# Optimization experiments

Measured on AMD Instinct MI355X. Metric: run time of the kernel, lower is better.

## Reference

```python
import jax, jax.numpy as jnp
import numpy as np

DT = 0.01
OMEGA_MAX = 100.0


def setup_inputs() -> dict:
    key = jax.random.key(0)
    ks = jax.random.split(key, 7)
    B, T, D, M = 4, 4096, 1024, 64
    N = 2 * M
    u = jax.random.normal(ks[0], (B, T, D), dtype=jnp.float32)
    W_omega = jax.random.normal(ks[1], (M, D), dtype=jnp.float32) * 0.02
    b_omega = jnp.ones((M,), dtype=jnp.float32)
    W_zeta = jax.random.normal(ks[2], (M, D), dtype=jnp.float32) * 0.02
    b_zeta = jnp.zeros((M,), dtype=jnp.float32)
    W_B = jax.random.normal(ks[3], (N, D), dtype=jnp.float32) * (0.1 / np.sqrt(D))
    b_B = jnp.zeros((N,), dtype=jnp.float32)
    C = jax.random.normal(ks[4], (D, N), dtype=jnp.float32) * 0.01
    D_mat = jax.random.normal(ks[5], (D, D), dtype=jnp.float32) * 0.01
    return dict(u=u, W_omega=W_omega, b_omega=b_omega, W_zeta=W_zeta,
                b_zeta=b_zeta, W_B=W_B, b_B=b_B, C=C, D_mat=D_mat)


def reference(u, W_omega, b_omega, W_zeta, b_zeta, W_B, b_B, C, D_mat):
    B, T, D = u.shape
    M = W_omega.shape[0]
    # Hoist all per-step linear projections into batched GEMMs (same math).
    omega = jax.nn.softplus(jnp.einsum('btd,md->btm', u, W_omega) + b_omega)
    omega = jnp.clip(omega, 1e-4, OMEGA_MAX)                      # (B,T,M)
    zeta = jax.nn.sigmoid(jnp.einsum('btd,md->btm', u, W_zeta) + b_zeta)
    A = omega * omega                                             # (B,T,M)
    S = 1.0 / (1.0 + (DT * DT) * A)                               # (B,T,M)
    d = 1.0 - zeta                                                # (B,T,M)
    F = jnp.einsum('btd,nd->btn', u, W_B) + b_B                   # (B,T,2M)

    def step(x, inp):
        A_t, S_t, d_t, F_t = inp                                  # (B,M)x3, (B,2M)
        z = x[:, :M]
        y = x[:, M:]
        z_new = d_t * (S_t * z - DT * A_t * S_t * y)
        y_new = d_t * (DT * S_t * z + S_t * y)
        x_new = jnp.concatenate([z_new, y_new], axis=-1) + F_t
        return x_new, x_new

    x0 = jnp.zeros((B, 2 * M), dtype=u.dtype)
    tm = lambda a: jnp.swapaxes(a, 0, 1)  # to time-major for scan
    _, xs = jax.lax.scan(step, x0, (tm(A), tm(S), tm(d), tm(F)))
    xs = jnp.swapaxes(xs, 0, 1)                                   # (B,T,2M)
    # Output projection: y_t = x_t C^T + u_t D^T
    y = jnp.einsum('btn,dn->btd', xs, C) + jnp.einsum('bte,de->btd', u, D_mat)
    return y
```

## Files before the change

kernel.cpp:

```cpp
#include <hip/hip_runtime.h>
#include <hip/hip_bf16.h>
#include <math.h>

#define DTC 0.01f

typedef __attribute__((ext_vector_type(8))) short short8;
typedef __attribute__((ext_vector_type(4))) float f32x4;
typedef unsigned short bf16raw;

__device__ __forceinline__ bf16raw f2bf(float f){
  union { unsigned u; float f; } v; v.f = f;
  unsigned r = v.u + 0x7FFF + ((v.u >> 16) & 1u);
  return (bf16raw)(r >> 16);
}

__device__ __forceinline__ short8 ld8f(const float* __restrict__ p){
  float4 a = *(const float4*)p;
  float4 b = *(const float4*)(p + 4);
  short8 r;
  r[0] = (short)f2bf(a.x); r[1] = (short)f2bf(a.y);
  r[2] = (short)f2bf(a.z); r[3] = (short)f2bf(a.w);
  r[4] = (short)f2bf(b.x); r[5] = (short)f2bf(b.y);
  r[6] = (short)f2bf(b.z); r[7] = (short)f2bf(b.w);
  return r;
}

template<int ITERS>
__device__ __forceinline__ void stage_async(const bf16raw* __restrict__ src, long ld,
                                            long row0, int k0, bf16raw* lds,
                                            int wave, int lane){
  int kchunk = (lane & 3) ^ ((lane >> 3) & 3);
#pragma unroll
  for (int i = 0; i < ITERS; ++i){
    int r0 = (wave*ITERS + i) * 16;
    long row = row0 + r0 + (lane >> 2);
    const bf16raw* gp = src + row*ld + k0 + kchunk*8;
    bf16raw* lp = lds + r0*32;
    __builtin_amdgcn_global_load_lds((const __attribute__((address_space(1))) void*)gp,
                                     (__attribute__((address_space(3))) void*)lp,
                                     16, 0, 0);
  }
}

template<int NI>
__device__ __forceinline__ void mma_tile(const bf16raw* Alds, const bf16raw* Blds,
                                         f32x4 acc[4][NI], int wm, int wn, int quad, int t16){
  short8 af[4], bfr[NI];
  int sw = (quad ^ ((t16 >> 1) & 3)) * 8;
#pragma unroll
  for (int mi = 0; mi < 4; ++mi)
    af[mi] = *(const short8*)(Alds + (wm*64 + mi*16 + t16)*32 + sw);
#pragma unroll
  for (int ni = 0; ni < NI; ++ni)
    bfr[ni] = *(const short8*)(Blds + (wn*(NI*16) + ni*16 + t16)*32 + sw);
#pragma unroll
  for (int mi = 0; mi < 4; ++mi)
#pragma unroll
    for (int ni = 0; ni < NI; ++ni)
      acc[mi][ni] = __builtin_amdgcn_mfma_f32_16x16x32_bf16(af[mi], bfr[ni], acc[mi][ni], 0, 0, 0);
}

extern "C" __global__ void k_prep(const float* __restrict__ u,
    const float* __restrict__ Wom, const float* __restrict__ Wze,
    const float* __restrict__ WB, const float* __restrict__ Cm,
    const float* __restrict__ Dm, bf16raw* __restrict__ u_bf,
    bf16raw* __restrict__ Wcat, bf16raw* __restrict__ C_bf,
    bf16raw* __restrict__ Dm_bf){
  long g = (long)blockIdx.x * 256 + threadIdx.x;
  const float* src; bf16raw* dst; long o;
  if      (g < 2097152){ src = u;   dst = u_bf;          o = g; }
  else if (g < 2105344){ src = Wom; dst = Wcat;          o = g - 2097152; }
  else if (g < 2113536){ src = Wze; dst = Wcat + 65536;  o = g - 2105344; }
  else if (g < 2129920){ src = WB;  dst = Wcat + 131072; o = g - 2113536; }
  else if (g < 2146304){ src = Cm;  dst = C_bf;          o = g - 2129920; }
  else                 { src = Dm;  dst = Dm_bf;         o = g - 2146304; }
  *(short8*)(dst + o*8) = ld8f(src + o*8);
}

extern "C" __global__ __launch_bounds__(256) void k_gemm_p(
    const bf16raw* __restrict__ u_bf, const bf16raw* __restrict__ Wcat,
    float* __restrict__ P){
  __shared__ __align__(16) bf16raw Alds[2][128*32];
  __shared__ __align__(16) bf16raw Blds[2][128*32];
  int tid = threadIdx.x, wave = tid >> 6, lane = tid & 63;
  int quad = lane >> 4, t16 = lane & 15;
  int wm = wave >> 1, wn = wave & 1;
  int id  = blockIdx.y * gridDim.x + blockIdx.x;
  int sid = (id & 7) * 32 + (id >> 3);
  long row0 = (long)(sid >> 1) * 128;
  int  col0 = (sid & 1) * 128;
  f32x4 acc[4][4] = {};

  auto stage = [&](int kt, int buf){
    stage_async<2>(u_bf, 1024, row0, kt*32, Alds[buf], wave, lane);
    stage_async<2>(Wcat, 1024, col0, kt*32, Blds[buf], wave, lane);
  };

  stage(0, 0);
  stage(1, 1);
  for (int kt = 0; kt < 30; ++kt){
    asm volatile("s_waitcnt vmcnt(4)" ::: "memory");
    __builtin_amdgcn_s_barrier();
    __builtin_amdgcn_sched_barrier(0);
    __builtin_amdgcn_s_setprio(1);
    mma_tile<4>(Alds[kt & 1], Blds[kt & 1], acc, wm, wn, quad, t16);
    __builtin_amdgcn_s_setprio(0);
    __builtin_amdgcn_sched_barrier(0);
    __builtin_amdgcn_s_barrier();
    stage(kt + 2, kt & 1);
  }
  asm volatile("s_waitcnt vmcnt(4)" ::: "memory");
  __builtin_amdgcn_s_barrier();
  __builtin_amdgcn_sched_barrier(0);
  mma_tile<4>(Alds[0], Blds[0], acc, wm, wn, quad, t16);
  asm volatile("s_waitcnt vmcnt(0)" ::: "memory");
  __builtin_amdgcn_s_barrier();
  __builtin_amdgcn_sched_barrier(0);
  mma_tile<4>(Alds[1], Blds[1], acc, wm, wn, quad, t16);
#pragma unroll
  for (int mi = 0; mi < 4; ++mi)
#pragma unroll
    for (int ni = 0; ni < 4; ++ni)
#pragma unroll
      for (int r = 0; r < 4; ++r){
        long grow = row0 + wm*64 + mi*16 + quad*4 + r;
        int  gcol = col0 + wn*64 + ni*16 + t16;
        P[grow*256 + gcol] = acc[mi][ni][r];
      }
}

extern "C" __global__ __launch_bounds__(256, 2) void k_gemm_out(
    const bf16raw* __restrict__ Xs, const bf16raw* __restrict__ u_bf,
    const bf16raw* __restrict__ C_bf, const bf16raw* __restrict__ Dm_bf,
    float* __restrict__ out){
  __shared__ __align__(16) bf16raw Alds[2][128*32];
  __shared__ __align__(16) bf16raw Blds[2][256*32];
  int tid = threadIdx.x, wave = tid >> 6, lane = tid & 63;
  int quad = lane >> 4, t16 = lane & 15;
  int wm = wave >> 1, wn = wave & 1;
  int id  = blockIdx.y * gridDim.x + blockIdx.x;
  int sid = (id & 7) * 64 + (id >> 3);
  long row0 = (long)(sid >> 2) * 128;
  int  col0 = (sid & 3) * 256;
  f32x4 acc[4][8] = {};

  auto stage = [&](int s, int buf){
    if (s < 4){
      stage_async<2>(Xs,   128, row0, s*32, Alds[buf], wave, lane);
      stage_async<4>(C_bf, 128, col0, s*32, Blds[buf], wave, lane);
    } else {
      stage_async<2>(u_bf,  1024, row0, (s-4)*32, Alds[buf], wave, lane);
      stage_async<4>(Dm_bf, 1024, col0, (s-4)*32, Blds[buf], wave, lane);
    }
  };

  stage(0, 0);
  stage(1, 1);
  for (int s = 0; s < 34; ++s){
    asm volatile("s_waitcnt vmcnt(6)" ::: "memory");
    __builtin_amdgcn_s_barrier();
    __builtin_amdgcn_sched_barrier(0);
    __builtin_amdgcn_s_setprio(1);
    mma_tile<8>(Alds[s & 1], Blds[s & 1], acc, wm, wn, quad, t16);
    __builtin_amdgcn_s_setprio(0);
    __builtin_amdgcn_sched_barrier(0);
    __builtin_amdgcn_s_barrier();
    stage(s + 2, s & 1);
  }
  asm volatile("s_waitcnt vmcnt(6)" ::: "memory");
  __builtin_amdgcn_s_barrier();
  __builtin_amdgcn_sched_barrier(0);
  mma_tile<8>(Alds[0], Blds[0], acc, wm, wn, quad, t16);
  asm volatile("s_waitcnt vmcnt(0)" ::: "memory");
  __builtin_amdgcn_s_barrier();
  __builtin_amdgcn_sched_barrier(0);
  mma_tile<8>(Alds[1], Blds[1], acc, wm, wn, quad, t16);
#pragma unroll
  for (int mi = 0; mi < 4; ++mi)
#pragma unroll
    for (int ni = 0; ni < 8; ++ni)
#pragma unroll
      for (int r = 0; r < 4; ++r){
        long grow = row0 + wm*64 + mi*16 + quad*4 + r;
        int  gcol = col0 + wn*128 + ni*16 + t16;
        out[grow*1024 + gcol] = acc[mi][ni][r];
      }
}

extern "C" __global__ __launch_bounds__(256) void k_scanA(
    const float* __restrict__ P, const float* __restrict__ b_om,
    const float* __restrict__ b_ze, const float* __restrict__ b_B,
    float4* __restrict__ Coef, float4* __restrict__ CM, float2* __restrict__ CV){
  int tid = threadIdx.x, c = blockIdx.x;
  int b = tid >> 6, m = tid & 63;
  float bo = b_om[m], bz = b_ze[m], bb0 = b_B[m], bb1 = b_B[64 + m];
  const float* row = P + ((size_t)b*4096 + c*16) * 256;
  float4* cf = Coef + ((size_t)b*4096 + c*16) * 64 + m;
  float m00=1.f, m01=0.f, m10=0.f, m11=0.f, vz=0.f, vy=0.f;
#pragma unroll 4
  for (int t = 0; t < 16; ++t){
    const float* r = row + t*256;
    float wo = r[m]       + bo;
    float wz = r[64 + m]  + bz;
    float fz = r[128 + m] + bb0;
    float fy = r[192 + m] + bb1;
    float sp = (wo > 20.f) ? wo : log1pf(expf(wo));
    float omega = fminf(fmaxf(sp, 1e-4f), 100.f);
    float A = omega * omega;
    float S = 1.f / (1.f + DTC*DTC*A);
    float zeta = 1.f / (1.f + expf(-wz));
    float p = (1.f - zeta) * S;
    float q = p * DTC * A;
    cf[t*64] = make_float4(p, q, fz, fy);
    float nvz = p*vz - q*vy + fz;
    float nvy = DTC*p*vz + p*vy + fy;
    vz = nvz; vy = nvy;
    float n00 = p*m00 - q*m10;
    float n01 = p*m01 - q*m11;
    float n10 = DTC*p*m00 + p*m10;
    float n11 = DTC*p*m01 + p*m11;
    m00=n00; m01=n01; m10=n10; m11=n11;
  }
  CM[c*256 + tid] = make_float4(m00, m01, m10, m11);
  CV[c*256 + tid] = make_float2(vz, vy);
}

extern "C" __global__ __launch_bounds__(256) void k_scanC(
    const float4* __restrict__ Coef, const float4* __restrict__ CM,
    const float2* __restrict__ CV, bf16raw* __restrict__ Xs){
  int tid = threadIdx.x, c = blockIdx.x;
  int b = tid >> 6, m = tid & 63;
  float xz = 0.f, xy = 0.f;
#pragma unroll 4
  for (int j = 0; j < c; ++j){
    float4 Mv = CM[j*256 + tid];
    float2 Vv = CV[j*256 + tid];
    float nz = Mv.x*xz + Mv.y*xy + Vv.x;
    float ny = Mv.z*xz + Mv.w*xy + Vv.y;
    xz = nz; xy = ny;
  }
  const float4* cf = Coef + ((size_t)b*4096 + c*16) * 64 + m;
  bf16raw* xp = Xs + ((size_t)b*4096 + c*16) * 128 + m;
#pragma unroll 4
  for (int t = 0; t < 16; ++t){
    float4 f = cf[t*64];
    float nz = f.x*xz - f.y*xy + f.z;
    float ny = DTC*f.x*xz + f.x*xy + f.w;
    xz = nz; xy = ny;
    xp[t*128]      = f2bf(xz);
    xp[t*128 + 64] = f2bf(xy);
  }
}

extern "C" void kernel_launch(void* const* d_in, const int* in_sizes, int n_in,
                              void* d_out, int out_size, void* d_ws, size_t ws_size,
                              hipStream_t stream){
  const float* u   = (const float*)d_in[0];
  const float* Wom = (const float*)d_in[1];
  const float* bom = (const float*)d_in[2];
  const float* Wze = (const float*)d_in[3];
  const float* bze = (const float*)d_in[4];
  const float* WB  = (const float*)d_in[5];
  const float* bB  = (const float*)d_in[6];
  const float* Cm  = (const float*)d_in[7];
  const float* Dm  = (const float*)d_in[8];
  float* out = (float*)d_out;

  char* ws = (char*)d_ws;
  size_t off = 0;
  bf16raw* u_bf  = (bf16raw*)(ws + off); off += (size_t)16777216*2;
  bf16raw* Wcat  = (bf16raw*)(ws + off); off += (size_t)262144*2;
  bf16raw* C_bf  = (bf16raw*)(ws + off); off += (size_t)131072*2;
  bf16raw* Dm_bf = (bf16raw*)(ws + off); off += (size_t)1048576*2;
  float*   P     = (float*)  (ws + off);
  bf16raw* Xs    = (bf16raw*)P;
  off += (size_t)16384*256*4;
  float4*  Coef  = (float4*) (ws + off); off += (size_t)16384*64*16;
  float4*  CMw   = (float4*) (ws + off); off += (size_t)256*256*16;
  float2*  CVw   = (float2*) (ws + off); off += (size_t)256*256*8;

  k_prep    <<<8896, 256, 0, stream>>>(u, Wom, Wze, WB, Cm, Dm, u_bf, Wcat, C_bf, Dm_bf);
  k_gemm_p  <<<dim3(2, 128), 256, 0, stream>>>(u_bf, Wcat, P);
  k_scanA   <<<256, 256, 0, stream>>>(P, bom, bze, bB, Coef, CMw, CVw);
  k_scanC   <<<256, 256, 0, stream>>>(Coef, CMw, CVw, Xs);
  k_gemm_out<<<dim3(4, 128), 256, 0, stream>>>(Xs, u_bf, C_bf, Dm_bf, out);
}
```

Baseline: 236.5 us.

## Triple-buffer LDS in both GEMMs and halve k_gemm_p M-tile

Both GEMM kernels move from double-buffered to triple-buffered LDS staging. The next async global-to-LDS load is issued before the MFMA work, which removes the second barrier in each k-iteration. k_gemm_p also shrinks its row tile from 128 to 64 and doubles the grid to 512 blocks, giving better CU coverage for a GEMM with few columns. The cost is more LDS per block, which could lower occupancy for k_gemm_out, and less operand reuse per block in k_gemm_p.

Result: faster. 231.5 us (-2.1%).

```diff
diff --git a/kernel.cpp b/kernel.cpp
--- a/kernel.cpp
+++ b/kernel.cpp
@@ -42,19 +42,19 @@
   }
 }
 
-template<int NI>
+template<int MI, int NI>
 __device__ __forceinline__ void mma_tile(const bf16raw* Alds, const bf16raw* Blds,
-                                         f32x4 acc[4][NI], int wm, int wn, int quad, int t16){
-  short8 af[4], bfr[NI];
+                                         f32x4 acc[MI][NI], int wm, int wn, int quad, int t16){
+  short8 af[MI], bfr[NI];
   int sw = (quad ^ ((t16 >> 1) & 3)) * 8;
 #pragma unroll
-  for (int mi = 0; mi < 4; ++mi)
-    af[mi] = *(const short8*)(Alds + (wm*64 + mi*16 + t16)*32 + sw);
+  for (int mi = 0; mi < MI; ++mi)
+    af[mi] = *(const short8*)(Alds + (wm*(MI*16) + mi*16 + t16)*32 + sw);
 #pragma unroll
   for (int ni = 0; ni < NI; ++ni)
     bfr[ni] = *(const short8*)(Blds + (wn*(NI*16) + ni*16 + t16)*32 + sw);
 #pragma unroll
-  for (int mi = 0; mi < 4; ++mi)
+  for (int mi = 0; mi < MI; ++mi)
 #pragma unroll
     for (int ni = 0; ni < NI; ++ni)
       acc[mi][ni] = __builtin_amdgcn_mfma_f32_16x16x32_bf16(af[mi], bfr[ni], acc[mi][ni], 0, 0, 0);
@@ -80,50 +80,51 @@
 extern "C" __global__ __launch_bounds__(256) void k_gemm_p(
     const bf16raw* __restrict__ u_bf, const bf16raw* __restrict__ Wcat,
     float* __restrict__ P){
-  __shared__ __align__(16) bf16raw Alds[2][128*32];
-  __shared__ __align__(16) bf16raw Blds[2][128*32];
+  __shared__ __align__(16) bf16raw Alds[3*64*32];
+  __shared__ __align__(16) bf16raw Blds[3*128*32];
   int tid = threadIdx.x, wave = tid >> 6, lane = tid & 63;
   int quad = lane >> 4, t16 = lane & 15;
   int wm = wave >> 1, wn = wave & 1;
   int id  = blockIdx.y * gridDim.x + blockIdx.x;
-  int sid = (id & 7) * 32 + (id >> 3);
-  long row0 = (long)(sid >> 1) * 128;
+  int sid = (id & 7) * 64 + (id >> 3);
+  long row0 = (long)(sid >> 1) * 64;
   int  col0 = (sid & 1) * 128;
-  f32x4 acc[4][4] = {};
+  f32x4 acc[2][4] = {};
 
   auto stage = [&](int kt, int buf){
-    stage_async<2>(u_bf, 1024, row0, kt*32, Alds[buf], wave, lane);
-    stage_async<2>(Wcat, 1024, col0, kt*32, Blds[buf], wave, lane);
+    stage_async<1>(u_bf, 1024, row0, kt*32, Alds + buf*(64*32), wave, lane);
+    stage_async<2>(Wcat, 1024, col0, kt*32, Blds + buf*(128*32), wave, lane);
   };
 
   stage(0, 0);
   stage(1, 1);
-  for (int kt = 0; kt < 30; ++kt){
-    asm volatile("s_waitcnt vmcnt(4)" ::: "memory");
+  int rd = 0;
+  for (int s = 0; s < 30; ++s){
+    asm volatile("s_waitcnt vmcnt(3)" ::: "memory");
     __builtin_amdgcn_s_barrier();
     __builtin_amdgcn_sched_barrier(0);
+    int st = rd >= 1 ? rd - 1 : 2;
+    stage(s + 2, st);
     __builtin_amdgcn_s_setprio(1);
-    mma_tile<4>(Alds[kt & 1], Blds[kt & 1], acc, wm, wn, quad, t16);
+    mma_tile<2,4>(Alds + rd*(64*32), Blds + rd*(128*32), acc, wm, wn, quad, t16);
     __builtin_amdgcn_s_setprio(0);
-    __builtin_amdgcn_sched_barrier(0);
-    __builtin_amdgcn_s_barrier();
-    stage(kt + 2, kt & 1);
-  }
-  asm volatile("s_waitcnt vmcnt(4)" ::: "memory");
-  __builtin_amdgcn_s_barrier();
-  __builtin_amdgcn_sched_barrier(0);
-  mma_tile<4>(Alds[0], Blds[0], acc, wm, wn, quad, t16);
+    rd = rd < 2 ? rd + 1 : 0;
+  }
+  asm volatile("s_waitcnt vmcnt(3)" ::: "memory");
+  __builtin_amdgcn_s_barrier();
+  __builtin_amdgcn_sched_barrier(0);
+  mma_tile<2,4>(Alds + 0*(64*32), Blds + 0*(128*32), acc, wm, wn, quad, t16);
   asm volatile("s_waitcnt vmcnt(0)" ::: "memory");
   __builtin_amdgcn_s_barrier();
   __builtin_amdgcn_sched_barrier(0);
-  mma_tile<4>(Alds[1], Blds[1], acc, wm, wn, quad, t16);
-#pragma unroll
-  for (int mi = 0; mi < 4; ++mi)
+  mma_tile<2,4>(Alds + 1*(64*32), Blds + 1*(128*32), acc, wm, wn, quad, t16);
+#pragma unroll
+  for (int mi = 0; mi < 2; ++mi)
 #pragma unroll
     for (int ni = 0; ni < 4; ++ni)
 #pragma unroll
       for (int r = 0; r < 4; ++r){
-        long grow = row0 + wm*64 + mi*16 + quad*4 + r;
+        long grow = row0 + wm*32 + mi*16 + quad*4 + r;
         int  gcol = col0 + wn*64 + ni*16 + t16;
         P[grow*256 + gcol] = acc[mi][ni][r];
       }
@@ -133,8 +134,8 @@
     const bf16raw* __restrict__ Xs, const bf16raw* __restrict__ u_bf,
     const bf16raw* __restrict__ C_bf, const bf16raw* __restrict__ Dm_bf,
     float* __restrict__ out){
-  __shared__ __align__(16) bf16raw Alds[2][128*32];
-  __shared__ __align__(16) bf16raw Blds[2][256*32];
+  __shared__ __align__(16) bf16raw Alds[3*128*32];
+  __shared__ __align__(16) bf16raw Blds[3*256*32];
   int tid = threadIdx.x, wave = tid >> 6, lane = tid & 63;
   int quad = lane >> 4, t16 = lane & 15;
   int wm = wave >> 1, wn = wave & 1;
@@ -146,35 +147,36 @@
 
   auto stage = [&](int s, int buf){
     if (s < 4){
-      stage_async<2>(Xs,   128, row0, s*32, Alds[buf], wave, lane);
-      stage_async<4>(C_bf, 128, col0, s*32, Blds[buf], wave, lane);
+      stage_async<2>(Xs,   128, row0, s*32, Alds + buf*(128*32), wave, lane);
+      stage_async<4>(C_bf, 128, col0, s*32, Blds + buf*(256*32), wave, lane);
     } else {
-      stage_async<2>(u_bf,  1024, row0, (s-4)*32, Alds[buf], wave, lane);
-      stage_async<4>(Dm_bf, 1024, col0, (s-4)*32, Blds[buf], wave, lane);
+      stage_async<2>(u_bf,  1024, row0, (s-4)*32, Alds + buf*(128*32), wave, lane);
+      stage_async<4>(Dm_bf, 1024, col0, (s-4)*32, Blds + buf*(256*32), wave, lane);
     }
   };
 
   stage(0, 0);
   stage(1, 1);
+  int rd = 0;
   for (int s = 0; s < 34; ++s){
     asm volatile("s_waitcnt vmcnt(6)" ::: "memory");
     __builtin_amdgcn_s_barrier();
     __builtin_amdgcn_sched_barrier(0);
+    int st = rd >= 1 ? rd - 1 : 2;
+    stage(s + 2, st);
     __builtin_amdgcn_s_setprio(1);
-    mma_tile<8>(Alds[s & 1], Blds[s & 1], acc, wm, wn, quad, t16);
+    mma_tile<4,8>(Alds + rd*(128*32), Blds + rd*(256*32), acc, wm, wn, quad, t16);
     __builtin_amdgcn_s_setprio(0);
-    __builtin_amdgcn_sched_barrier(0);
-    __builtin_amdgcn_s_barrier();
-    stage(s + 2, s & 1);
+    rd = rd < 2 ? rd + 1 : 0;
   }
   asm volatile("s_waitcnt vmcnt(6)" ::: "memory");
   __builtin_amdgcn_s_barrier();
   __builtin_amdgcn_sched_barrier(0);
-  mma_tile<8>(Alds[0], Blds[0], acc, wm, wn, quad, t16);
+  mma_tile<4,8>(Alds + 1*(128*32), Blds + 1*(256*32), acc, wm, wn, quad, t16);
   asm volatile("s_waitcnt vmcnt(0)" ::: "memory");
   __builtin_amdgcn_s_barrier();
   __builtin_amdgcn_sched_barrier(0);
-  mma_tile<8>(Alds[1], Blds[1], acc, wm, wn, quad, t16);
+  mma_tile<4,8>(Alds + 2*(128*32), Blds + 2*(256*32), acc, wm, wn, quad, t16);
 #pragma unroll
   for (int mi = 0; mi < 4; ++mi)
 #pragma unroll
@@ -280,7 +282,7 @@
   float2*  CVw   = (float2*) (ws + off); off += (size_t)256*256*8;
 
   k_prep    <<<8896, 256, 0, stream>>>(u, Wom, Wze, WB, Cm, Dm, u_bf, Wcat, C_bf, Dm_bf);
-  k_gemm_p  <<<dim3(2, 128), 256, 0, stream>>>(u_bf, Wcat, P);
+  k_gemm_p  <<<dim3(2, 256), 256, 0, stream>>>(u_bf, Wcat, P);
   k_scanA   <<<256, 256, 0, stream>>>(P, bom, bze, bB, Coef, CMw, CVw);
   k_scanC   <<<256, 256, 0, stream>>>(Coef, CMw, CVw, Xs);
   k_gemm_out<<<dim3(4, 128), 256, 0, stream>>>(Xs, u_bf, C_bf, Dm_bf, out);
```
